# Kernel tuning notes

Measured on AMD Instinct MI355X. Metric: run time of the kernel, lower is better.

## Reference

```python
import jax, jax.numpy as jnp
import numpy as np

N = 65536  # number of points
# (out_ch, in_ch) for the 8 shared-MLP (1x1-conv) blocks
_DIMS = [(64, 3), (64, 64), (128, 64), (1024, 128), (512, 1088), (256, 512), (128, 256), (1, 128)]


def setup_inputs() -> dict:
    key = jax.random.key(0)
    ks = jax.random.split(key, 1 + 2 * len(_DIMS))
    inp = {"x": jax.random.normal(ks[0], (1, 1, N, 3), jnp.float32)}
    for i, (o, c) in enumerate(_DIMS):
        scale = 1.0 / np.sqrt(c)
        inp[f"W{i+1}"] = jax.random.normal(ks[1 + 2 * i], (o, c), jnp.float32) * scale
        inp[f"b{i+1}"] = jax.random.uniform(ks[2 + 2 * i], (o,), jnp.float32, -scale, scale)
    return inp


def reference(x, W1, b1, W2, b2, W3, b3, W4, b4, W5, b5, W6, b6, W7, b7, W8, b8):
    # x: [1,1,n,3]. Conv2d with kernel [1,3] over the width-3 axis == per-point linear on xyz.
    pts = x[0, 0]                                   # [n,3]
    n = pts.shape[0]
    h = jax.nn.relu(pts @ W1.T + b1)                # [n,64]   block1
    h = jax.nn.relu(h @ W2.T + b2)                  # [n,64]   block2 (kept for skip-concat)
    y = jax.nn.relu(h @ W3.T + b3)                  # [n,128]  block3
    y = jax.nn.relu(y @ W4.T + b4)                  # [n,1024] block4
    g = jnp.max(y, axis=0)                          # [1024]   global max-pool over points
    # broadcast global feature to every point and concat with per-point features -> [n,1088]
    feat = jnp.concatenate([h, jnp.broadcast_to(g, (n, g.shape[0]))], axis=1)
    z = jax.nn.relu(feat @ W5.T + b5)               # [n,512]
    z = jax.nn.relu(z @ W6.T + b6)                  # [n,256]
    z = jax.nn.relu(z @ W7.T + b7)                  # [n,128]
    z = z @ W8.T + b8                               # [n,1]    block8 (no relu)
    return z.reshape(1, 1, n, 1)
```

## Files before the change

### kernel.cpp

```cpp
#include <hip/hip_runtime.h>

#define NPTS 65536

typedef __bf16 bf16_t;
typedef __bf16 bf16x8 __attribute__((ext_vector_type(8)));
typedef float f32x16 __attribute__((ext_vector_type(16)));

#define MFMA32(A, B, C) __builtin_amdgcn_mfma_f32_32x32x16_bf16(A, B, C, 0, 0, 0)

__device__ __forceinline__ float relu(float v) { return v > 0.f ? v : 0.f; }


struct PrepSeg { const float* src; bf16_t* h; bf16_t* l; int SW; int K; int nblk; };
struct PrepAll { PrepSeg seg[6]; };

__global__ __launch_bounds__(256) void kprep(PrepAll pa) {
  int blk = blockIdx.x, i = 0;
  while (blk >= pa.seg[i].nblk) { blk -= pa.seg[i].nblk; ++i; }
  const PrepSeg sg = pa.seg[i];
  int t8 = blk * 256 + threadIdx.x;
  int l = t8 & 63;
  int rest = t8 >> 6;
  int NKC = sg.K >> 4;
  int kc = rest % NKC, st = rest / NKC;
  int n = st * 32 + (l & 31);
  int k0 = kc * 16 + (l >> 5) * 8;
  const float* src = sg.src + (size_t)n * sg.SW + k0;
  bf16x8 hv, lv;
#pragma unroll
  for (int j = 0; j < 8; ++j) {
    float v = src[j];
    bf16_t h = (bf16_t)v;
    hv[j] = h; lv[j] = (bf16_t)(v - (float)h);
  }
  *(bf16x8*)(sg.h + (size_t)t8 * 8) = hv;
  *(bf16x8*)(sg.l + (size_t)t8 * 8) = lv;
}

__global__ __launch_bounds__(256, 2) void k1a(
    const float* __restrict__ x, const float* __restrict__ W1, const float* __restrict__ b1,
    bf16_t* __restrict__ h1h, bf16_t* __restrict__ h1l) {
  int p = blockIdx.x * 256 + threadIdx.x;
  float x0 = x[p * 3 + 0], x1 = x[p * 3 + 1], x2 = x[p * 3 + 2];
  int b = p >> 7, mi = (p >> 5) & 3, p31 = p & 31;
#pragma unroll
  for (int kc = 0; kc < 4; ++kc)
#pragma unroll
    for (int hbw = 0; hbw < 2; ++hbw) {
      bf16x8 hv, lv;
#pragma unroll
      for (int j = 0; j < 8; ++j) {
        int c = kc * 16 + hbw * 8 + j;
        float v = relu(fmaf(W1[c * 3], x0, fmaf(W1[c * 3 + 1], x1, fmaf(W1[c * 3 + 2], x2, b1[c]))));
        bf16_t h = (bf16_t)v;
        hv[j] = h; lv[j] = (bf16_t)(v - (float)h);
      }
      size_t off = (((size_t)(b * 4 + kc) * 4 + mi) * 64 + hbw * 32 + p31) * 8;
      *(bf16x8*)(h1h + off) = hv;
      *(bf16x8*)(h1l + off) = lv;
    }
}

struct Oct { bf16x8 h0, l0, h1, l1; };
__device__ __forceinline__ Oct epi_pack(const f32x16& accv, int hb) {
  float a[16], rcv[8];
#pragma unroll
  for (int r = 0; r < 16; ++r) a[r] = relu(accv[r]);
#pragma unroll
  for (int j = 0; j < 8; ++j) rcv[j] = __shfl_xor(hb ? a[j] : a[8 + j], 32);
  float o0[8], o1[8];
#pragma unroll
  for (int j = 0; j < 4; ++j) {
    o0[j]     = hb ? rcv[j]     : a[j];
    o0[4 + j] = hb ? a[8 + j]   : rcv[j];
    o1[j]     = hb ? rcv[4 + j] : a[4 + j];
    o1[4 + j] = hb ? a[12 + j]  : rcv[4 + j];
  }
  Oct o;
#pragma unroll
  for (int j = 0; j < 8; ++j) {
    bf16_t x0 = (bf16_t)o0[j]; o.h0[j] = x0; o.l0[j] = (bf16_t)(o0[j] - (float)x0);
    bf16_t x1 = (bf16_t)o1[j]; o.h1[j] = x1; o.l1[j] = (bf16_t)(o1[j] - (float)x1);
  }
  return o;
}

__device__ __forceinline__ void epi_store_lds(const Oct& o, bf16_t* H, bf16_t* L, int ob, int p31) {
  *(bf16x8*)(H + (ob + p31) * 8)      = o.h0;
  *(bf16x8*)(H + (ob + 32 + p31) * 8) = o.h1;
  *(bf16x8*)(L + (ob + p31) * 8)      = o.l0;
  *(bf16x8*)(L + (ob + 32 + p31) * 8) = o.l1;
}

__device__ __forceinline__ void binit2(f32x16 acc[2], const float* bias, int base, int hb) {
#pragma unroll
  for (int r = 0; r < 16; ++r) {
    float bv = bias[base + 8 * (r >> 2) + 4 * hb + (r & 3)];
    acc[0][r] = bv; acc[1][r] = bv;
  }
}

template <int PB, int K, int MODE>
__global__ __launch_bounds__(256, 3) void gemmS(
    const bf16_t* __restrict__ Ah, const bf16_t* __restrict__ Al,
    const bf16_t* __restrict__ Wh, const bf16_t* __restrict__ Wl,
    const float* __restrict__ bias, int nko,
    bf16_t* __restrict__ Oh, bf16_t* __restrict__ Ol,
    float* __restrict__ aux, const float* __restrict__ w8, const float* __restrict__ b8) {
  constexpr int WC = 4 / PB;
  constexpr int NKC = K / 16;
  constexpr int KG = 2;
  constexpr int NG = NKC / KG;
  __shared__ bf16_t smem[2][PB][2][KG * 2048];

  int tid = threadIdx.x;
  int lane = tid & 63;
  int w = __builtin_amdgcn_readfirstlane(tid >> 6);
  int rg = w / WC, cw = w % WC;
  int hb = lane >> 5, p31 = lane & 31;
  int bx = blockIdx.x;
  int st0 = blockIdx.y * WC + cw;
  int bblk = bx * PB + rg;

  f32x16 acc[4];
#pragma unroll
  for (int r = 0; r < 16; ++r) {
    float bv = bias[st0 * 32 + 8 * (r >> 2) + 4 * hb + (r & 3)];
#pragma unroll
    for (int mi = 0; mi < 4; ++mi) acc[mi][r] = bv;
  }

  auto stage = [&](int buf, int g) {
#pragma unroll
    for (int i = 0; i < PB * 4; ++i) {
      int u = i * 256 + tid;
      int rgs = u >> 10, rem = u & 1023;
      int t = rem >> 9, inner = rem & 511;
      const bf16_t* src = (t ? Al : Ah) +
          ((size_t)(bx * PB + rgs) * NKC + g * KG) * 2048 + inner * 8;
      *(bf16x8*)&smem[buf][rgs][t][inner * 8] = *(const bf16x8*)src;
    }
  };

  bf16x8 wch[KG], wcl[KG], wnh[KG], wnl[KG];
  auto wload = [&](int g, bf16x8* h, bf16x8* l) {
#pragma unroll
    for (int kcl = 0; kcl < KG; ++kcl) {
      size_t wo = (((size_t)st0 * NKC + g * KG + kcl) * 64 + lane) * 8;
      h[kcl] = *(const bf16x8*)(Wh + wo);
      l[kcl] = *(const bf16x8*)(Wl + wo);
    }
  };

  auto compute = [&](int buf, bf16x8* h, bf16x8* l) {
#pragma unroll
    for (int kcl = 0; kcl < KG; ++kcl)
#pragma unroll
      for (int mi = 0; mi < 4; ++mi) {
        const bf16_t* xp = &smem[buf][rg][0][((kcl * 4 + mi) * 64 + lane) * 8];
        bf16x8 xh = *(const bf16x8*)xp;
        bf16x8 xl = *(const bf16x8*)(xp + KG * 2048);
        acc[mi] = MFMA32(h[kcl], xh, acc[mi]);
        acc[mi] = MFMA32(l[kcl], xh, acc[mi]);
        acc[mi] = MFMA32(h[kcl], xl, acc[mi]);
      }
  };

  stage(0, 0);
  wload(0, wch, wcl);
  for (int g = 0; g < NG; ++g) {
    __syncthreads();
    if (g + 1 < NG) {
      stage((g + 1) & 1, g + 1);
      wload(g + 1, wnh, wnl);
    }
    compute(g & 1, wch, wcl);
#pragma unroll
    for (int kcl = 0; kcl < KG; ++kcl) { wch[kcl] = wnh[kcl]; wcl[kcl] = wnl[kcl]; }
  }

  if constexpr (MODE == 0) {
#pragma unroll
    for (int mi = 0; mi < 4; ++mi) {
      Oct o = epi_pack(acc[mi], hb);
      int kco = st0 * 2 + hb;
      size_t ob = ((size_t)(bblk * nko + kco) * 4 + mi) * 64;
      *(bf16x8*)(Oh + (ob + p31) * 8)      = o.h0;
      *(bf16x8*)(Ol + (ob + p31) * 8)      = o.l0;
      *(bf16x8*)(Oh + (ob + 32 + p31) * 8) = o.h1;
      *(bf16x8*)(Ol + (ob + 32 + p31) * 8) = o.l1;
    }
  } else if constexpr (MODE == 1) {
#pragma unroll
    for (int r = 0; r < 16; ++r) {
      float m = relu(acc[0][r]);
#pragma unroll
      for (int mi = 1; mi < 4; ++mi) m = fmaxf(m, relu(acc[mi][r]));
#pragma unroll
      for (int off = 1; off < 32; off <<= 1) m = fmaxf(m, __shfl_xor(m, off));
      if (p31 == 0)
        aux[(size_t)bx * 1024 + st0 * 32 + 8 * (r >> 2) + 4 * hb + (r & 3)] = m;
    }
  } else {
    __shared__ float sp[4][128];
    float w8v[16];
#pragma unroll
    for (int r = 0; r < 16; ++r) w8v[r] = w8[st0 * 32 + 8 * (r >> 2) + 4 * hb + (r & 3)];
#pragma unroll
    for (int mi = 0; mi < 4; ++mi) {
      float s = 0.f;
#pragma unroll
      for (int r = 0; r < 16; ++r) s = fmaf(relu(acc[mi][r]), w8v[r], s);
      s += __shfl_xor(s, 32);
      if (hb == 0) sp[w][mi * 32 + p31] = s;
    }
    __syncthreads();
    if (tid < 128)
      aux[(size_t)bx * 128 + tid] = sp[0][tid] + sp[1][tid] + sp[2][tid] + sp[3][tid] + b8[0];
  }
}

__global__ __launch_bounds__(512, 1) void kl34max(
    const bf16_t* __restrict__ h2h, const bf16_t* __restrict__ h2l,
    const bf16_t* __restrict__ W3h, const bf16_t* __restrict__ W3l,
    const float* __restrict__ b3,
    const bf16_t* __restrict__ Wh, const bf16_t* __restrict__ Wl,
    const float* __restrict__ bias, float* __restrict__ gpart) {
  __shared__ __align__(16) bf16_t sA[81920];
  bf16_t* wq = sA + 65536;
  int tid = threadIdx.x, lane = tid & 63;
  int w = __builtin_amdgcn_readfirstlane(tid >> 6);
  int w3 = w & 3, t = w >> 2;
  int sslot = w >> 1, part = w & 1;
  int hb = lane >> 5, p31 = lane & 31;
  int bx = blockIdx.x;
  int pb = bx * 2 + t;
  int rot = (bx >> 2) & 7;
  bf16_t* sT = sA + t * 32768;

  bf16x8 hx[4], lx[4];
#pragma unroll
  for (int kc = 0; kc < 4; ++kc) {
    size_t so = (((size_t)(pb * 4 + kc) * 4 + w3) * 64 + lane) * 8;
    hx[kc] = *(const bf16x8*)(h2h + so);
    lx[kc] = *(const bf16x8*)(h2l + so);
  }
#pragma unroll
  for (int spr = 0; spr < 2; ++spr) {
    f32x16 a3[2];
#pragma unroll
    for (int s = 0; s < 2; ++s) {
      int st = spr * 2 + s;
#pragma unroll
      for (int r = 0; r < 16; ++r)
        a3[s][r] = b3[st * 32 + 8 * (r >> 2) + 4 * hb + (r & 3)];
    }
#pragma unroll
    for (int kc = 0; kc < 4; ++kc)
#pragma unroll
      for (int s = 0; s < 2; ++s) {
        int st = spr * 2 + s;
        size_t wo = ((size_t)(st * 4 + kc) * 64 + lane) * 8;
        bf16x8 wh3 = *(const bf16x8*)(W3h + wo);
        bf16x8 wl3 = *(const bf16x8*)(W3l + wo);
        a3[s] = MFMA32(wh3, hx[kc], a3[s]);
        a3[s] = MFMA32(wl3, hx[kc], a3[s]);
        a3[s] = MFMA32(wh3, lx[kc], a3[s]);
      }
#pragma unroll
    for (int s = 0; s < 2; ++s) {
      int st = spr * 2 + s;
      Oct o = epi_pack(a3[s], hb);
      epi_store_lds(o, sT, sT + 16384, ((st * 2 + hb) * 4 + w3) * 64, p31);
    }
  }
  __syncthreads();

  auto issueS = [&](int u) {
    int jj = u >> 3, kc = u & 7;
    int st = ((jj + rot) & 7) * 4 + sslot;
    const bf16_t* W = part ? Wl : Wh;
    const bf16_t* gp = W + ((size_t)(st * 8 + kc) * 64 + lane) * 8;
    bf16_t* lp = wq + (u & 3) * 4096 + sslot * 1024 + part * 512;
    __builtin_amdgcn_global_load_lds(
        (const __attribute__((address_space(1))) void*)gp,
        (__attribute__((address_space(3))) void*)lp, 16, 0, 0);
  };
  issueS(0); issueS(1); issueS(2);

  f32x16 acc[4];
#pragma unroll 1
  for (int u = 0; u < 64; ++u) {
    if (u <= 61)      asm volatile("s_waitcnt vmcnt(2)" ::: "memory");
    else if (u == 62) asm volatile("s_waitcnt vmcnt(1)" ::: "memory");
    else              asm volatile("s_waitcnt vmcnt(0)" ::: "memory");
    __builtin_amdgcn_sched_barrier(0);
    __builtin_amdgcn_s_barrier();
    if (u + 3 < 64) issueS(u + 3);
    int jj = u >> 3, kc = u & 7;
    int st = ((jj + rot) & 7) * 4 + w3;
    if (kc == 0) {
#pragma unroll
      for (int r = 0; r < 16; ++r) {
        float bv = bias[st * 32 + 8 * (r >> 2) + 4 * hb + (r & 3)];
#pragma unroll
        for (int mi = 0; mi < 4; ++mi) acc[mi][r] = bv;
      }
    }
    const bf16_t* wb = wq + (u & 3) * 4096 + w3 * 1024;
    bf16x8 cwh = *(const bf16x8*)(wb + lane * 8);
    bf16x8 cwl = *(const bf16x8*)(wb + 512 + lane * 8);
    __builtin_amdgcn_s_setprio(1);
#pragma unroll
    for (int mi = 0; mi < 4; ++mi) {
      const bf16_t* xp = sT + ((kc * 4 + mi) * 64 + lane) * 8;
      bf16x8 xh = *(const bf16x8*)xp;
      bf16x8 xl = *(const bf16x8*)(xp + 16384);
      acc[mi] = MFMA32(cwh, xh, acc[mi]);
      acc[mi] = MFMA32(cwl, xh, acc[mi]);
      acc[mi] = MFMA32(cwh, xl, acc[mi]);
    }
    __builtin_amdgcn_s_setprio(0);
    if (kc == 7) {
#pragma unroll
      for (int r = 0; r < 16; ++r) {
        float m = fmaxf(fmaxf(acc[0][r], acc[1][r]), fmaxf(acc[2][r], acc[3][r]));
        m = fmaxf(m, 0.f);
#pragma unroll
        for (int off = 1; off < 32; off <<= 1) m = fmaxf(m, __shfl_xor(m, off));
        if (p31 == 0)
          __builtin_nontemporal_store(
              m, gpart + (size_t)pb * 1024 + st * 32 + 8 * (r >> 2) + 4 * hb + (r & 3));
      }
    }
  }
}

__global__ __launch_bounds__(256) void kgmax(const float* __restrict__ gpart, float* __restrict__ g) {
  int t = blockIdx.x * 256 + threadIdx.x;
  int c = t & 1023, rg = t >> 10;
  const float* gp = gpart + (size_t)rg * 64 * 1024 + c;
  float m = 0.f;
#pragma unroll 8
  for (int r = 0; r < 64; ++r) m = fmaxf(m, gp[(size_t)r * 1024]);
  atomicMax((unsigned int*)(g + c), __float_as_uint(m));
}

__global__ __launch_bounds__(256) void kc5(
    const float* __restrict__ W5, const float* __restrict__ b5,
    const float* __restrict__ g, float* __restrict__ c5) {
  int tid = threadIdx.x;
  int ci = tid >> 3, kg = tid & 7;
  int c = blockIdx.x * 32 + ci;
  const float* wrow = W5 + (size_t)c * 1088 + 64 + kg * 128;
  const float* gp = g + kg * 128;
  float acc = 0.f;
#pragma unroll 8
  for (int k = 0; k < 128; ++k) acc += wrow[k] * gp[k];
#pragma unroll
  for (int off = 1; off <= 4; off <<= 1) acc += __shfl_xor(acc, off);
  if (kg == 0) c5[c] = acc + b5[c];
}


__global__ __launch_bounds__(256, 2) void mega2(
    const bf16_t* __restrict__ h2gh, const bf16_t* __restrict__ h2gl,
    const bf16_t* __restrict__ W5h, const bf16_t* __restrict__ W5l, const float* __restrict__ c5,
    const bf16_t* __restrict__ W6h, const bf16_t* __restrict__ W6l, const float* __restrict__ b6,
    const bf16_t* __restrict__ W7h, const bf16_t* __restrict__ W7l, const float* __restrict__ b7,
    const float* __restrict__ w8, const float* __restrict__ b8v, float* __restrict__ out) {
  __shared__ __align__(16) bf16_t smem[32768];
  __shared__ float sp[4][64];
  int tid = threadIdx.x, lane = tid & 63;
  int w = __builtin_amdgcn_readfirstlane(tid >> 6);
  int hb = lane >> 5, p31 = lane & 31;
  int b = blockIdx.x;
  int B = b >> 1, half = b & 1;

  bf16x8 xh[4][2], xl[4][2];
#pragma unroll
  for (int kc = 0; kc < 4; ++kc)
#pragma unroll
    for (int mi = 0; mi < 2; ++mi) {
      size_t so = (((size_t)((B * 4 + kc) * 4 + half * 2 + mi)) * 64 + lane) * 8;
      xh[kc][mi] = *(const bf16x8*)(h2gh + so);
      xl[kc][mi] = *(const bf16x8*)(h2gl + so);
    }

  f32x16 z6a[2][2];
#pragma unroll
  for (int s = 0; s < 2; ++s)
#pragma unroll
    for (int r = 0; r < 16; ++r) {
      float bv = b6[(w * 2 + s) * 32 + 8 * (r >> 2) + 4 * hb + (r & 3)];
      z6a[s][0][r] = bv; z6a[s][1][r] = bv;
    }

  bf16x8 w5h[4], w5l[4];
  auto w5load = [&](int g) {
#pragma unroll
    for (int kc = 0; kc < 4; ++kc) {
      size_t wo = (((size_t)(g * 4 + w) * 4 + kc) * 64 + lane) * 8;
      w5h[kc] = *(const bf16x8*)(W5h + wo);
      w5l[kc] = *(const bf16x8*)(W5l + wo);
    }
  };
  w5load(0);

  bf16x8 cwh[2], cwl[2], nwh[2], nwl[2];
  auto w6load = [&](int g, int kc, bf16x8* hh, bf16x8* ll) {
#pragma unroll
    for (int s = 0; s < 2; ++s) {
      size_t wo = ((size_t)((w * 2 + s) * 32 + g * 8 + kc) * 64 + lane) * 8;
      hh[s] = *(const bf16x8*)(W6h + wo);
      ll[s] = *(const bf16x8*)(W6l + wo);
    }
  };

  for (int g5 = 0; g5 < 4; ++g5) {
    bf16_t* zbuf = smem + (g5 & 1) * 16384;
    int st5 = g5 * 4 + w;
    f32x16 a5[2];
    binit2(a5, c5, st5 * 32, hb);
    __builtin_amdgcn_s_setprio(1);
#pragma unroll
    for (int kc = 0; kc < 4; ++kc) {
#pragma unroll
      for (int mi = 0; mi < 2; ++mi) a5[mi] = MFMA32(w5h[kc], xh[kc][mi], a5[mi]);
#pragma unroll
      for (int mi = 0; mi < 2; ++mi) a5[mi] = MFMA32(w5l[kc], xh[kc][mi], a5[mi]);
#pragma unroll
      for (int mi = 0; mi < 2; ++mi) a5[mi] = MFMA32(w5h[kc], xl[kc][mi], a5[mi]);
    }
    __builtin_amdgcn_s_setprio(0);
    if (g5 < 3) w5load(g5 + 1);
#pragma unroll
    for (int mi = 0; mi < 2; ++mi) {
      Oct o = epi_pack(a5[mi], hb);
      epi_store_lds(o, zbuf, zbuf + 8192, ((w * 2 + hb) * 2 + mi) * 64, p31);
    }
    w6load(g5, 0, cwh, cwl);
    __syncthreads();
#pragma unroll
    for (int kc = 0; kc < 8; ++kc) {
      if (kc < 7) w6load(g5, kc + 1, nwh, nwl);
      bf16x8 zxh[2], zxl[2];
#pragma unroll
      for (int mi = 0; mi < 2; ++mi) {
        const bf16_t* xp = zbuf + ((kc * 2 + mi) * 64 + lane) * 8;
        zxh[mi] = *(const bf16x8*)xp;
        zxl[mi] = *(const bf16x8*)(xp + 8192);
      }
      __builtin_amdgcn_s_setprio(1);
#pragma unroll
      for (int s = 0; s < 2; ++s)
#pragma unroll
        for (int mi = 0; mi < 2; ++mi) z6a[s][mi] = MFMA32(cwh[s], zxh[mi], z6a[s][mi]);
#pragma unroll
      for (int s = 0; s < 2; ++s)
#pragma unroll
        for (int mi = 0; mi < 2; ++mi) z6a[s][mi] = MFMA32(cwl[s], zxh[mi], z6a[s][mi]);
#pragma unroll
      for (int s = 0; s < 2; ++s)
#pragma unroll
        for (int mi = 0; mi < 2; ++mi) z6a[s][mi] = MFMA32(cwh[s], zxl[mi], z6a[s][mi]);
      __builtin_amdgcn_s_setprio(0);
#pragma unroll
      for (int s = 0; s < 2; ++s) { cwh[s] = nwh[s]; cwl[s] = nwl[s]; }
    }
  }
  __syncthreads();
#pragma unroll
  for (int s = 0; s < 2; ++s) {
    int kcb = (w * 2 + s) * 2 + hb;
#pragma unroll
    for (int mi = 0; mi < 2; ++mi) {
      Oct o = epi_pack(z6a[s][mi], hb);
      epi_store_lds(o, smem, smem + 16384, (kcb * 2 + mi) * 64, p31);
    }
  }
  bf16x8 a7wh, a7wl, n7h, n7l;
  {
    size_t wo = ((size_t)(w * 16) * 64 + lane) * 8;
    a7wh = *(const bf16x8*)(W7h + wo);
    a7wl = *(const bf16x8*)(W7l + wo);
  }
  __syncthreads();
  f32x16 a7[2];
  binit2(a7, b7, w * 32, hb);
#pragma unroll
  for (int kc = 0; kc < 16; ++kc) {
    if (kc < 15) {
      size_t wo = ((size_t)(w * 16 + kc + 1) * 64 + lane) * 8;
      n7h = *(const bf16x8*)(W7h + wo);
      n7l = *(const bf16x8*)(W7l + wo);
    }
    bf16x8 zxh[2], zxl[2];
#pragma unroll
    for (int mi = 0; mi < 2; ++mi) {
      const bf16_t* xp = smem + ((kc * 2 + mi) * 64 + lane) * 8;
      zxh[mi] = *(const bf16x8*)xp;
      zxl[mi] = *(const bf16x8*)(xp + 16384);
    }
    __builtin_amdgcn_s_setprio(1);
#pragma unroll
    for (int mi = 0; mi < 2; ++mi) a7[mi] = MFMA32(a7wh, zxh[mi], a7[mi]);
#pragma unroll
    for (int mi = 0; mi < 2; ++mi) a7[mi] = MFMA32(a7wl, zxh[mi], a7[mi]);
#pragma unroll
    for (int mi = 0; mi < 2; ++mi) a7[mi] = MFMA32(a7wh, zxl[mi], a7[mi]);
    __builtin_amdgcn_s_setprio(0);
    a7wh = n7h; a7wl = n7l;
  }
  float w8v[16];
#pragma unroll
  for (int r = 0; r < 16; ++r) w8v[r] = w8[w * 32 + 8 * (r >> 2) + 4 * hb + (r & 3)];
#pragma unroll
  for (int mi = 0; mi < 2; ++mi) {
    float s = 0.f;
#pragma unroll
    for (int r = 0; r < 16; ++r) s = fmaf(relu(a7[mi][r]), w8v[r], s);
    s += __shfl_xor(s, 32);
    if (hb == 0) sp[w][mi * 32 + p31] = s;
  }
  __syncthreads();
  if (tid < 64)
    out[b * 64 + tid] = sp[0][tid] + sp[1][tid] + sp[2][tid] + sp[3][tid] + b8v[0];
}

extern "C" void kernel_launch(void* const* d_in, const int* in_sizes, int n_in,
                              void* d_out, int out_size, void* d_ws, size_t ws_size,
                              hipStream_t stream) {
  const float* x  = (const float*)d_in[0];
  const float* W1 = (const float*)d_in[1];  const float* b1 = (const float*)d_in[2];
  const float* W2 = (const float*)d_in[3];  const float* b2 = (const float*)d_in[4];
  const float* W3 = (const float*)d_in[5];  const float* b3 = (const float*)d_in[6];
  const float* W4 = (const float*)d_in[7];  const float* b4 = (const float*)d_in[8];
  const float* W5 = (const float*)d_in[9];  const float* b5 = (const float*)d_in[10];
  const float* W6 = (const float*)d_in[11]; const float* b6 = (const float*)d_in[12];
  const float* W7 = (const float*)d_in[13]; const float* b7 = (const float*)d_in[14];
  const float* W8 = (const float*)d_in[15]; const float* b8 = (const float*)d_in[16];
  float* out = (float*)d_out;

  const size_t MB = 1ull << 20;
  char* ws = (char*)d_ws;
  bf16_t* h2h = (bf16_t*)(ws + 128 * MB);  bf16_t* h2l = (bf16_t*)(ws + 136 * MB);
  bf16_t* h1h = (bf16_t*)(ws + 144 * MB);  bf16_t* h1l = (bf16_t*)(ws + 152 * MB);
  float* gpart = (float*)(ws + 208 * MB);
  float* g     = (float*)(ws + 210 * MB);
  float* c5    = (float*)(ws + 210 * MB + 4096);
  char* wb = ws + 210 * MB + 65536;
  bf16_t* W2h = (bf16_t*)(wb);             bf16_t* W2l = (bf16_t*)(wb + 8192);
  bf16_t* W3h = (bf16_t*)(wb + 16384);     bf16_t* W3l = (bf16_t*)(wb + 32768);
  bf16_t* W4h = (bf16_t*)(wb + 49152);     bf16_t* W4l = (bf16_t*)(wb + 311296);
  bf16_t* W5h = (bf16_t*)(wb + 573440);    bf16_t* W5l = (bf16_t*)(wb + 638976);
  bf16_t* W6h = (bf16_t*)(wb + 704512);    bf16_t* W6l = (bf16_t*)(wb + 966656);
  bf16_t* W7h = (bf16_t*)(wb + 1228800);   bf16_t* W7l = (bf16_t*)(wb + 1294336);

  hipMemsetAsync(g, 0, 1024 * sizeof(float), stream);

  PrepAll pa;
  pa.seg[0] = {W2, W2h, W2l, 64, 64, 2};
  pa.seg[1] = {W3, W3h, W3l, 64, 64, 4};
  pa.seg[2] = {W4, W4h, W4l, 128, 128, 64};
  pa.seg[3] = {W5, W5h, W5l, 1088, 64, 16};
  pa.seg[4] = {W6, W6h, W6l, 512, 512, 64};
  pa.seg[5] = {W7, W7h, W7l, 256, 256, 16};
  kprep<<<166, 256, 0, stream>>>(pa);

  k1a<<<256, 256, 0, stream>>>(x, W1, b1, h1h, h1l);
  gemmS<2, 64, 0><<<dim3(256, 1), 256, 0, stream>>>(
      h1h, h1l, W2h, W2l, b2, 4, h2h, h2l, nullptr, nullptr, nullptr);
  kl34max<<<256, 512, 0, stream>>>(h2h, h2l, W3h, W3l, b3, W4h, W4l, b4, gpart);
  kgmax<<<32, 256, 0, stream>>>(gpart, g);
  kc5<<<16, 256, 0, stream>>>(W5, b5, g, c5);
  mega2<<<1024, 256, 0, stream>>>(h2h, h2l, W5h, W5l, c5, W6h, W6l, b6,
                                  W7h, W7l, b7, W8, b8, out);
}
```

Before: 267.0 us.

## Give each wave its own double-buffered weight stream and drop per-step block barrier

In the layer-4 max-pool kernel, the block-shared 4-slot weight ring is replaced. Previously it was filled cooperatively and guarded by an s_barrier every step. Now each wave loads its own hi/lo weight tiles into a private two-slot LDS buffer, prefetching one step ahead. The goal is to remove block-wide synchronisation so waves can drift independently. In exchange, prefetch depth drops from three steps to one, and waves sharing the same w3 now load identical weights twice, doubling weight fetch traffic through L2. The nontemporal store of the partial max values is also replaced with a plain store.

```diff
diff --git a/kernel.cpp b/kernel.cpp
--- a/kernel.cpp
+++ b/kernel.cpp
@@ -231,12 +231,12 @@
   int tid = threadIdx.x, lane = tid & 63;
   int w = __builtin_amdgcn_readfirstlane(tid >> 6);
   int w3 = w & 3, t = w >> 2;
-  int sslot = w >> 1, part = w & 1;
   int hb = lane >> 5, p31 = lane & 31;
   int bx = blockIdx.x;
   int pb = bx * 2 + t;
   int rot = (bx >> 2) & 7;
   bf16_t* sT = sA + t * 32768;
+  bf16_t* wbuf = wq + w * 2048;
 
   bf16x8 hx[4], lx[4];
 #pragma unroll
@@ -276,27 +276,31 @@
   }
   __syncthreads();
 
-  auto issueS = [&](int u) {
+  auto issueW = [&](int u) {
     int jj = u >> 3, kc = u & 7;
-    int st = ((jj + rot) & 7) * 4 + sslot;
-    const bf16_t* W = part ? Wl : Wh;
-    const bf16_t* gp = W + ((size_t)(st * 8 + kc) * 64 + lane) * 8;
-    bf16_t* lp = wq + (u & 3) * 4096 + sslot * 1024 + part * 512;
+    int st = ((jj + rot) & 7) * 4 + w3;
+    const bf16_t* gph = Wh + ((size_t)(st * 8 + kc) * 64 + lane) * 8;
+    const bf16_t* gpl = Wl + ((size_t)(st * 8 + kc) * 64 + lane) * 8;
+    bf16_t* lp = wbuf + (u & 1) * 1024;
     __builtin_amdgcn_global_load_lds(
-        (const __attribute__((address_space(1))) void*)gp,
+        (const __attribute__((address_space(1))) void*)gph,
         (__attribute__((address_space(3))) void*)lp, 16, 0, 0);
+    __builtin_amdgcn_global_load_lds(
+        (const __attribute__((address_space(1))) void*)gpl,
+        (__attribute__((address_space(3))) void*)(lp + 512), 16, 0, 0);
   };
-  issueS(0); issueS(1); issueS(2);
+  issueW(0);
 
   f32x16 acc[4];
 #pragma unroll 1
   for (int u = 0; u < 64; ++u) {
-    if (u <= 61)      asm volatile("s_waitcnt vmcnt(2)" ::: "memory");
-    else if (u == 62) asm volatile("s_waitcnt vmcnt(1)" ::: "memory");
-    else              asm volatile("s_waitcnt vmcnt(0)" ::: "memory");
+    if (u + 1 < 64) {
+      issueW(u + 1);
+      asm volatile("s_waitcnt vmcnt(2)" ::: "memory");
+    } else {
+      asm volatile("s_waitcnt vmcnt(0)" ::: "memory");
+    }
     __builtin_amdgcn_sched_barrier(0);
-    __builtin_amdgcn_s_barrier();
-    if (u + 3 < 64) issueS(u + 3);
     int jj = u >> 3, kc = u & 7;
     int st = ((jj + rot) & 7) * 4 + w3;
     if (kc == 0) {
@@ -307,7 +311,7 @@
         for (int mi = 0; mi < 4; ++mi) acc[mi][r] = bv;
       }
     }
-    const bf16_t* wb = wq + (u & 3) * 4096 + w3 * 1024;
+    const bf16_t* wb = wbuf + (u & 1) * 1024;
     bf16x8 cwh = *(const bf16x8*)(wb + lane * 8);
     bf16x8 cwl = *(const bf16x8*)(wb + 512 + lane * 8);
     __builtin_amdgcn_s_setprio(1);
@@ -329,8 +333,7 @@
 #pragma unroll
         for (int off = 1; off < 32; off <<= 1) m = fmaxf(m, __shfl_xor(m, off));
         if (p31 == 0)
-          __builtin_nontemporal_store(
-              m, gpart + (size_t)pb * 1024 + st * 32 + 8 * (r >> 2) + 4 * hb + (r & 3));
+          gpart[(size_t)pb * 1024 + st * 32 + 8 * (r >> 2) + 4 * hb + (r & 3)] = m;
       }
     }
   }
```

Result: faster. 258.9 us (-3.0%).
